# Performance work log

Hardware: AMD Instinct MI355X
Metric: run time of the kernel (lower is better)

The kernel has to match this reference:

```python
import jax, jax.numpy as jnp
import numpy as np

B, S, H, P = 8, 2048, 256, 64
NQ = 20

def setup_inputs() -> dict:
    key = jax.random.key(0)
    ks = jax.random.split(key, 12)
    s = lambda fan_in: 1.0 / np.sqrt(fan_in)
    return {
        "feature_x": jax.random.normal(ks[0], (B, S, H), dtype=jnp.float32),
        "param_x": jax.random.normal(ks[1], (B, S, P), dtype=jnp.float32),
        "sim_w1": jax.random.uniform(ks[2], (H, H // 2), jnp.float32, -s(H), s(H)),
        "sim_b1": jax.random.uniform(ks[3], (H // 2,), jnp.float32, -s(H), s(H)),
        "sim_w2": jax.random.uniform(ks[4], (H // 2, 1), jnp.float32, -s(H // 2), s(H // 2)),
        "sim_b2": jax.random.uniform(ks[5], (1,), jnp.float32, -s(H // 2), s(H // 2)),
        "conf_w1": jax.random.uniform(ks[6], (H, H // 2), jnp.float32, -s(H), s(H)),
        "conf_b1": jax.random.uniform(ks[7], (H // 2,), jnp.float32, -s(H), s(H)),
        "conf_w2": jax.random.uniform(ks[8], (H // 2, 1), jnp.float32, -s(H // 2), s(H // 2)),
        "conf_b2": jax.random.uniform(ks[9], (1,), jnp.float32, -s(H // 2), s(H // 2)),
        "questions": jax.random.randint(ks[10], (B, S), 0, NQ, dtype=jnp.int64 if jax.config.jax_enable_x64 else jnp.int32),
    }

def _mlp_scalar(x, w1, b1, w2, b2):
    # [B,S,H] -> [B,S] (dropout is eval-mode identity)
    h = jax.nn.relu(jnp.einsum("bsh,hk->bsk", x, w1) + b1)
    return (jnp.einsum("bsk,ko->bso", h, w2) + b2)[..., 0]

def reference(feature_x, param_x, sim_w1, sim_b1, sim_w2, sim_b2,
              conf_w1, conf_b1, conf_w2, conf_b2, questions):
    similarities = _mlp_scalar(feature_x, sim_w1, sim_b1, sim_w2, sim_b2)          # [B,S]
    confidences = jax.nn.sigmoid(_mlp_scalar(feature_x, conf_w1, conf_b1, conf_w2, conf_b2))  # [B,S]
    # multiplicative equality mask (zeros, not -inf, outside group — faithful to source)
    qmask = (questions[:, :, None] == questions[:, None, :]).astype(feature_x.dtype)  # [B,S,S]
    logits = similarities[:, :, None] * qmask                                        # [B,i,j]
    attn = jax.nn.softmax(logits, axis=-2)                                           # softmax over i
    smoothed = jnp.einsum("bij,bip->bjp", attn, param_x)                              # attn^T @ param_x
    c = confidences[..., None]
    return c * param_x + (1.0 - c) * smoothed
```

## Files before the change

### kernel.cpp

```cpp
#include <hip/hip_runtime.h>
#include <math.h>

#define B_  8
#define S_  2048
#define H_  256
#define HK_ 128
#define P_  64
#define NQ_ 20
#define M_  (B_*S_)
#define ACC_STRIDE 2688

#define WS_SIM   0
#define WS_CONF  16384
#define WS_ACC   32768
#define WS_WT    54272

typedef __attribute__((ext_vector_type(8))) short bf16x8;
typedef __attribute__((ext_vector_type(4))) float f32x4;

__global__ void prep_kernel(const float* __restrict__ sw1, const float* __restrict__ cw1,
                            short* __restrict__ wtf, float* __restrict__ ws_acc)
{
    const int t = blockIdx.x * 256 + threadIdx.x;
    const int l = t & 63, nt = (t >> 6) & 7, kt = (t >> 9) & 7, mlp = t >> 12;
    const int col = l & 15, quad = l >> 4;
    const int n = nt * 16 + col;
    const float* w1 = mlp ? cw1 : sw1;
    short frag[8];
    #pragma unroll
    for (int j = 0; j < 8; ++j) {
        int k = kt * 32 + quad * 8 + j;
        union { float f; unsigned u; } c; c.f = w1[k * HK_ + n];
        frag[j] = (short)((c.u + 0x7FFF + ((c.u >> 16) & 1)) >> 16);
    }
    *(uint4*)(wtf + (size_t)t * 8) = *(const uint4*)frag;
    for (int s = t; s < B_ * ACC_STRIDE; s += 8192) ws_acc[s] = 0.f;
}

__launch_bounds__(256)
__global__ void mlp_mfma_kernel(const float* __restrict__ fx, const short* __restrict__ wtf,
                                const float* __restrict__ sb1, const float* __restrict__ sw2,
                                const float* __restrict__ sb2, const float* __restrict__ cb1,
                                const float* __restrict__ cw2, const float* __restrict__ cb2,
                                float* __restrict__ sim, float* __restrict__ conf)
{
    const int tid  = threadIdx.x;
    const int w    = tid >> 6, l = tid & 63;
    const int col  = l & 15, quad = l >> 4;
    const int mlp  = w >> 1, mt = w & 1;
    const int row  = blockIdx.x * 32 + mt * 16 + col;

    f32x4 acc[8];
    #pragma unroll
    for (int nt = 0; nt < 8; ++nt) acc[nt] = (f32x4){0.f, 0.f, 0.f, 0.f};

    const float* fxrow = fx + (size_t)row * H_;
    const short* wf = wtf + (size_t)mlp * 32768 + (size_t)l * 8;

    #pragma unroll
    for (int kt = 0; kt < 8; ++kt) {
        float4 a0 = *(const float4*)(fxrow + kt * 32 + quad * 8);
        float4 a1 = *(const float4*)(fxrow + kt * 32 + quad * 8 + 4);
        float af[8] = {a0.x, a0.y, a0.z, a0.w, a1.x, a1.y, a1.z, a1.w};
        bf16x8 ahi, alo;
        #pragma unroll
        for (int i = 0; i < 8; ++i) {
            union { float f; unsigned u; } c; c.f = af[i];
            unsigned hi = c.u >> 16;
            ahi[i] = (short)hi;
            union { float f; unsigned u; } h2; h2.u = hi << 16;
            union { float f; unsigned u; } c2; c2.f = af[i] - h2.f;
            alo[i] = (short)(c2.u >> 16);
        }
        const short* base = wf + (size_t)kt * 4096;
        #pragma unroll
        for (int nt = 0; nt < 8; ++nt) {
            bf16x8 bf = *(const bf16x8*)(base + nt * 512);
            acc[nt] = __builtin_amdgcn_mfma_f32_16x16x32_bf16(ahi, bf, acc[nt], 0, 0, 0);
            acc[nt] = __builtin_amdgcn_mfma_f32_16x16x32_bf16(alo, bf, acc[nt], 0, 0, 0);
        }
    }

    const float* b1 = mlp ? cb1 : sb1;
    const float* w2 = mlp ? cw2 : sw2;
    const float  b2v = mlp ? cb2[0] : sb2[0];
    float p[4] = {0.f, 0.f, 0.f, 0.f};
    #pragma unroll
    for (int nt = 0; nt < 8; ++nt) {
        float b1c = b1[nt * 16 + col];
        float w2c = w2[nt * 16 + col];
        #pragma unroll
        for (int j = 0; j < 4; ++j)
            p[j] += fmaxf(acc[nt][j] + b1c, 0.f) * w2c;
    }
    #pragma unroll
    for (int off = 8; off >= 1; off >>= 1)
        #pragma unroll
        for (int j = 0; j < 4; ++j) p[j] += __shfl_down(p[j], off, 16);

    if (col == 0) {
        #pragma unroll
        for (int j = 0; j < 4; ++j) {
            int r = blockIdx.x * 32 + mt * 16 + quad * 4 + j;
            float v = p[j] + b2v;
            if (mlp == 0) sim[r] = v;
            else          conf[r] = 1.0f / (1.0f + expf(-v));
        }
    }
}

__launch_bounds__(256)
__global__ void accum_kernel(const float* __restrict__ sim, const int* __restrict__ questions,
                             const float* __restrict__ px, float* __restrict__ ws_acc)
{
    const int b = blockIdx.x;
    const int chunk = blockIdx.y;
    const int tid = threadIdx.x;
    const int lane = tid & 63;
    const int g = tid >> 6;
    __shared__ float accs[4][ACC_STRIDE];
    for (int s = tid; s < 4 * ACC_STRIDE; s += 256) ((float*)accs)[s] = 0.f;
    __syncthreads();

    const float* simb = sim + b * S_;
    const int*   qb   = questions + b * S_;
    const float* pxb  = px + (size_t)b * S_ * P_;

    float Treg = 0.f;
    const int i0 = chunk * 64 + g;
    for (int t = 0; t < 16; ++t) {
        int i = i0 + 4 * t;
        int qi = qb[i];
        float e = expf(simb[i]);
        float v = pxb[(size_t)i * P_ + lane];
        Treg += v;
        accs[g][qi * 64 + lane]        += v;
        accs[g][(20 + qi) * 64 + lane] += e * v;
        if (lane == 0) {
            accs[g][2624 + qi] += e;
            accs[g][2644 + qi] += 1.0f;
        }
    }
    accs[g][2560 + lane] += Treg;
    __syncthreads();

    float* dst = ws_acc + (size_t)b * ACC_STRIDE;
    for (int s = tid; s < ACC_STRIDE; s += 256) {
        float sum = accs[0][s] + accs[1][s] + accs[2][s] + accs[3][s];
        atomicAdd(dst + s, sum);
    }
}

__global__ void output_kernel(const float* __restrict__ px, const float* __restrict__ conf,
                              const int* __restrict__ questions, const float* __restrict__ ws_acc,
                              float* __restrict__ out)
{
    const int idx = blockIdx.x * 256 + threadIdx.x;
    const int row = idx >> 4;
    const int p4  = idx & 15;
    const int b   = row >> 11;
    const float c = conf[row];
    const int   q = questions[row];
    const float* accb = ws_acc + (size_t)b * ACC_STRIDE;
    const float4 T = *(const float4*)(accb + 2560 + p4 * 4);
    const float4 G = *(const float4*)(accb + q * 64 + p4 * 4);
    const float4 E = *(const float4*)(accb + (20 + q) * 64 + p4 * 4);
    const float denom = ((float)S_ - accb[2644 + q]) + accb[2624 + q];
    const float inv = 1.0f / denom;
    const float4 pv = ((const float4*)px)[idx];
    const float om = 1.0f - c;
    float4 o;
    o.x = c * pv.x + om * ((T.x - G.x + E.x) * inv);
    o.y = c * pv.y + om * ((T.y - G.y + E.y) * inv);
    o.z = c * pv.z + om * ((T.z - G.z + E.z) * inv);
    o.w = c * pv.w + om * ((T.w - G.w + E.w) * inv);
    ((float4*)out)[idx] = o;
}

extern "C" void kernel_launch(void* const* d_in, const int* in_sizes, int n_in,
                              void* d_out, int out_size, void* d_ws, size_t ws_size,
                              hipStream_t stream) {
    const float* fx  = (const float*)d_in[0];
    const float* px  = (const float*)d_in[1];
    const float* sw1 = (const float*)d_in[2];
    const float* sb1 = (const float*)d_in[3];
    const float* sw2 = (const float*)d_in[4];
    const float* sb2 = (const float*)d_in[5];
    const float* cw1 = (const float*)d_in[6];
    const float* cb1 = (const float*)d_in[7];
    const float* cw2 = (const float*)d_in[8];
    const float* cb2 = (const float*)d_in[9];
    const int* questions = (const int*)d_in[10];
    float* out = (float*)d_out;

    float* ws     = (float*)d_ws;
    float* sim    = ws + WS_SIM;
    float* conf   = ws + WS_CONF;
    float* ws_acc = ws + WS_ACC;
    short* wtf    = (short*)(ws + WS_WT);

    prep_kernel<<<32, 256, 0, stream>>>(sw1, cw1, wtf, ws_acc);
    mlp_mfma_kernel<<<M_ / 32, 256, 0, stream>>>(fx, wtf, sb1, sw2, sb2,
                                                 cb1, cw2, cb2, sim, conf);
    accum_kernel<<<dim3(B_, 32), 256, 0, stream>>>(sim, questions, px, ws_acc);
    output_kernel<<<(M_ * P_ / 4) / 256, 256, 0, stream>>>(px, conf, questions,
                                                           ws_acc, out);
}
```

Measured before the change: 110.4 us.

## Fuse MLP scoring with group accumulation and replicate global accumulators

Merges the accumulation kernel into the MLP kernel, so similarity scores stay in shared memory and each block accumulates its own 32 rows into a shared histogram using LDS atomics. The per-block partials are added into NREP replicated global accumulator copies, skipping zero entries, to reduce contention among 512 blocks. The output kernel then sums the replicas. This removes one launch and the sim round trip, but adds global atomics from many more blocks and LDS atomic contention.

```diff
diff --git a/kernel.cpp b/kernel.cpp
--- a/kernel.cpp
+++ b/kernel.cpp
@@ -9,11 +9,11 @@
 #define NQ_ 20
 #define M_  (B_*S_)
 #define ACC_STRIDE 2688
-
-#define WS_SIM   0
-#define WS_CONF  16384
-#define WS_ACC   32768
-#define WS_WT    54272
+#define NREP 4
+
+#define WS_CONF  0
+#define WS_ACC   16384
+#define WS_WT    (16384 + NREP*B_*ACC_STRIDE)
 
 typedef __attribute__((ext_vector_type(8))) short bf16x8;
 typedef __attribute__((ext_vector_type(4))) float f32x4;
@@ -34,17 +34,23 @@
         frag[j] = (short)((c.u + 0x7FFF + ((c.u >> 16) & 1)) >> 16);
     }
     *(uint4*)(wtf + (size_t)t * 8) = *(const uint4*)frag;
-    for (int s = t; s < B_ * ACC_STRIDE; s += 8192) ws_acc[s] = 0.f;
+    for (int s = t; s < NREP * B_ * ACC_STRIDE; s += 8192) ws_acc[s] = 0.f;
 }
 
 __launch_bounds__(256)
-__global__ void mlp_mfma_kernel(const float* __restrict__ fx, const short* __restrict__ wtf,
-                                const float* __restrict__ sb1, const float* __restrict__ sw2,
-                                const float* __restrict__ sb2, const float* __restrict__ cb1,
-                                const float* __restrict__ cw2, const float* __restrict__ cb2,
-                                float* __restrict__ sim, float* __restrict__ conf)
+__global__ void mlp_accum_kernel(const float* __restrict__ fx, const short* __restrict__ wtf,
+                                 const float* __restrict__ sb1, const float* __restrict__ sw2,
+                                 const float* __restrict__ sb2, const float* __restrict__ cb1,
+                                 const float* __restrict__ cw2, const float* __restrict__ cb2,
+                                 const float* __restrict__ px, const int* __restrict__ questions,
+                                 float* __restrict__ conf, float* __restrict__ ws_acc)
 {
+    __shared__ float accs[ACC_STRIDE];
+    __shared__ float sim_l[32];
+
     const int tid  = threadIdx.x;
+    for (int s = tid; s < ACC_STRIDE; s += 256) accs[s] = 0.f;
+
     const int w    = tid >> 6, l = tid & 63;
     const int col  = l & 15, quad = l >> 4;
     const int mlp  = w >> 1, mt = w & 1;
@@ -101,53 +107,40 @@
     if (col == 0) {
         #pragma unroll
         for (int j = 0; j < 4; ++j) {
-            int r = blockIdx.x * 32 + mt * 16 + quad * 4 + j;
+            int rloc = mt * 16 + quad * 4 + j;
             float v = p[j] + b2v;
-            if (mlp == 0) sim[r] = v;
-            else          conf[r] = 1.0f / (1.0f + expf(-v));
-        }
-    }
-}
-
-__launch_bounds__(256)
-__global__ void accum_kernel(const float* __restrict__ sim, const int* __restrict__ questions,
-                             const float* __restrict__ px, float* __restrict__ ws_acc)
-{
-    const int b = blockIdx.x;
-    const int chunk = blockIdx.y;
-    const int tid = threadIdx.x;
-    const int lane = tid & 63;
-    const int g = tid >> 6;
-    __shared__ float accs[4][ACC_STRIDE];
-    for (int s = tid; s < 4 * ACC_STRIDE; s += 256) ((float*)accs)[s] = 0.f;
+            if (mlp == 0) sim_l[rloc] = v;
+            else          conf[blockIdx.x * 32 + rloc] = 1.0f / (1.0f + expf(-v));
+        }
+    }
     __syncthreads();
 
-    const float* simb = sim + b * S_;
-    const int*   qb   = questions + b * S_;
-    const float* pxb  = px + (size_t)b * S_ * P_;
-
+    const int row0 = blockIdx.x * 32;
     float Treg = 0.f;
-    const int i0 = chunk * 64 + g;
-    for (int t = 0; t < 16; ++t) {
-        int i = i0 + 4 * t;
-        int qi = qb[i];
-        float e = expf(simb[i]);
-        float v = pxb[(size_t)i * P_ + lane];
+    #pragma unroll
+    for (int t = 0; t < 8; ++t) {
+        const int il = w + 4 * t;
+        const int i  = row0 + il;
+        const int qi = questions[i];
+        const float e = expf(sim_l[il]);
+        const float v = px[(size_t)i * P_ + l];
         Treg += v;
-        accs[g][qi * 64 + lane]        += v;
-        accs[g][(20 + qi) * 64 + lane] += e * v;
-        if (lane == 0) {
-            accs[g][2624 + qi] += e;
-            accs[g][2644 + qi] += 1.0f;
-        }
-    }
-    accs[g][2560 + lane] += Treg;
+        atomicAdd(&accs[qi * 64 + l], v);
+        atomicAdd(&accs[(20 + qi) * 64 + l], e * v);
+        if (l == 0) {
+            atomicAdd(&accs[2624 + qi], e);
+            atomicAdd(&accs[2644 + qi], 1.0f);
+        }
+    }
+    atomicAdd(&accs[2560 + l], Treg);
     __syncthreads();
 
-    float* dst = ws_acc + (size_t)b * ACC_STRIDE;
+    const int b   = blockIdx.x >> 6;
+    const int rep = blockIdx.x & (NREP - 1);
+    float* dst = ws_acc + (size_t)(b * NREP + rep) * ACC_STRIDE;
     for (int s = tid; s < ACC_STRIDE; s += 256) {
-        float sum = accs[0][s] + accs[1][s] + accs[2][s] + accs[3][s];
-        atomicAdd(dst + s, sum);
+        const float vv = accs[s];
+        if (vv != 0.f) atomicAdd(dst + s, vv);
     }
 }
 
@@ -161,19 +154,31 @@
     const int b   = row >> 11;
     const float c = conf[row];
     const int   q = questions[row];
-    const float* accb = ws_acc + (size_t)b * ACC_STRIDE;
-    const float4 T = *(const float4*)(accb + 2560 + p4 * 4);
-    const float4 G = *(const float4*)(accb + q * 64 + p4 * 4);
-    const float4 E = *(const float4*)(accb + (20 + q) * 64 + p4 * 4);
-    const float denom = ((float)S_ - accb[2644 + q]) + accb[2624 + q];
+
+    float Tx=0.f,Ty=0.f,Tz=0.f,Tw=0.f;
+    float Gx=0.f,Gy=0.f,Gz=0.f,Gw=0.f;
+    float Ex=0.f,Ey=0.f,Ez=0.f,Ew=0.f;
+    float Wq=0.f, nq=0.f;
+    #pragma unroll
+    for (int rep = 0; rep < NREP; ++rep) {
+        const float* a = ws_acc + (size_t)(b * NREP + rep) * ACC_STRIDE;
+        const float4 t4 = *(const float4*)(a + 2560 + p4 * 4);
+        const float4 g4 = *(const float4*)(a + q * 64 + p4 * 4);
+        const float4 e4 = *(const float4*)(a + (20 + q) * 64 + p4 * 4);
+        Tx += t4.x; Ty += t4.y; Tz += t4.z; Tw += t4.w;
+        Gx += g4.x; Gy += g4.y; Gz += g4.z; Gw += g4.w;
+        Ex += e4.x; Ey += e4.y; Ez += e4.z; Ew += e4.w;
+        Wq += a[2624 + q]; nq += a[2644 + q];
+    }
+    const float denom = ((float)S_ - nq) + Wq;
     const float inv = 1.0f / denom;
     const float4 pv = ((const float4*)px)[idx];
     const float om = 1.0f - c;
     float4 o;
-    o.x = c * pv.x + om * ((T.x - G.x + E.x) * inv);
-    o.y = c * pv.y + om * ((T.y - G.y + E.y) * inv);
-    o.z = c * pv.z + om * ((T.z - G.z + E.z) * inv);
-    o.w = c * pv.w + om * ((T.w - G.w + E.w) * inv);
+    o.x = c * pv.x + om * ((Tx - Gx + Ex) * inv);
+    o.y = c * pv.y + om * ((Ty - Gy + Ey) * inv);
+    o.z = c * pv.z + om * ((Tz - Gz + Ez) * inv);
+    o.w = c * pv.w + om * ((Tw - Gw + Ew) * inv);
     ((float4*)out)[idx] = o;
 }
 
@@ -194,15 +199,14 @@
     float* out = (float*)d_out;
 
     float* ws     = (float*)d_ws;
-    float* sim    = ws + WS_SIM;
     float* conf   = ws + WS_CONF;
     float* ws_acc = ws + WS_ACC;
     short* wtf    = (short*)(ws + WS_WT);
 
     prep_kernel<<<32, 256, 0, stream>>>(sw1, cw1, wtf, ws_acc);
-    mlp_mfma_kernel<<<M_ / 32, 256, 0, stream>>>(fx, wtf, sb1, sw2, sb2,
-                                                 cb1, cw2, cb2, sim, conf);
-    accum_kernel<<<dim3(B_, 32), 256, 0, stream>>>(sim, questions, px, ws_acc);
+    mlp_accum_kernel<<<M_ / 32, 256, 0, stream>>>(fx, wtf, sb1, sw2, sb2,
+                                                  cb1, cw2, cb2, px, questions,
+                                                  conf, ws_acc);
     output_kernel<<<(M_ * P_ / 4) / 256, 256, 0, stream>>>(px, conf, questions,
                                                            ws_acc, out);
 }
```

Result: slower. 115.2 us (+4.3%).
